# Performance work log

Hardware: AMD Instinct MI355X
Metric: run time of the kernel (lower is better)

Reference implementation:

```python
import jax, jax.numpy as jnp
import numpy as np

# gaussian_radial_function width: gamma = 1/(2*sigma^2), sigma = radii spacing (2/7)
GAMMA = 6.125


def setup_inputs() -> dict:
    key = jax.random.key(0)
    k1, k2, k3, k4, k5 = jax.random.split(key, 5)
    n, b, a, c, d, r = 4, 256, 256, 16, 16, 8
    inp = jax.random.normal(k1, (n, c, a), dtype=jnp.float32)
    difference_mat = jax.random.normal(k2, (n, b, a, 3), dtype=jnp.float32)
    relative_mask = jax.random.uniform(k3, (n, b, a), dtype=jnp.float32)
    W = jax.random.normal(k4, (d, c, r), dtype=jnp.float32) / np.float32(np.sqrt(c * r))
    radii = jax.random.uniform(k5, (r,), dtype=jnp.float32) * 2.0
    return {"input": inp, "difference_mat": difference_mat,
            "relative_mask": relative_mask, "W": W, "radii": radii}


def reference(input, difference_mat, relative_mask, W, radii):
    # distances |x_b - x_a|: [n, b, a]
    dist = jnp.sqrt(jnp.sum(difference_mat * difference_mat, axis=-1))
    # gaussian radial basis: [n, b, a, r]
    R = jnp.exp(-GAMMA * (dist[..., None] - radii) ** 2)
    # apply relative mask (kernel = mask[n,b,a] * kernel[d,c,n,b,a] in original)
    R = R * relative_mask[..., None]
    # kernel[d,c,n,b,a] = sum_r W[d,c,r] * R[n,b,a,r]; fused with the
    # contraction 'nca,dcnba->ndb' into a single einsum.
    return jnp.einsum('nca,dcr,nbar->ndb', input, W, R)
```

## Files before the change

### kernel.cpp

```cpp
#include <hip/hip_runtime.h>
#include <math.h>

constexpr int N = 4, B = 256, A = 256, C = 16, D = 16, RR = 8;
constexpr int DR = D * RR;
constexpr int BT = 4;
constexpr float GAMMA = 6.125f;

__global__ __launch_bounds__(256) void se3_compute_P(
    const float* __restrict__ input, const float* __restrict__ W,
    float* __restrict__ P)
{
    const int blk = blockIdx.x;
    const int n  = blk / DR;
    const int dr = blk % DR;
    const int d  = dr / RR;
    const int r  = dr % RR;
    const int a  = threadIdx.x;

    float s = 0.f;
#pragma unroll
    for (int c = 0; c < C; ++c) {
        s += W[(d * C + c) * RR + r] * input[(n * C + c) * A + a];
    }
    P[(size_t)blk * A + a] = s;
}

__global__ __launch_bounds__(256) void se3_compute_out(
    const float* __restrict__ P, const float* __restrict__ diff,
    const float* __restrict__ mask, const float* __restrict__ radii,
    float* __restrict__ out)
{
    const int blk = blockIdx.x;
    const int n  = blk / (B / BT);
    const int b0 = (blk % (B / BT)) * BT;
    const int a  = threadIdx.x;
    const int lane = threadIdx.x & 63;
    const int wave = threadIdx.x >> 6;

    float rad[RR];
#pragma unroll
    for (int r = 0; r < RR; ++r) rad[r] = radii[r];

    float preg[DR];
    const float* Pn = P + (size_t)n * DR * A + a;
#pragma unroll
    for (int dr = 0; dr < DR; ++dr) preg[dr] = Pn[dr * A];

    __shared__ float lds[BT][4][D];

#pragma unroll
    for (int bi = 0; bi < BT; ++bi) {
        const int b = b0 + bi;
        const size_t nba = (size_t)(n * B + b) * A + a;
        const float* dp = diff + nba * 3;
        const float dx = dp[0], dy = dp[1], dz = dp[2];
        const float dist = sqrtf(dx * dx + dy * dy + dz * dz);
        const float m = mask[nba];

        float R[RR];
#pragma unroll
        for (int r = 0; r < RR; ++r) {
            const float t = dist - rad[r];
            R[r] = m * __expf(-GAMMA * t * t);
        }

        float acc[D];
#pragma unroll
        for (int d = 0; d < D; ++d) {
            float s = 0.f;
#pragma unroll
            for (int r = 0; r < RR; ++r) s += R[r] * preg[d * RR + r];
            acc[d] = s;
        }

        {
            const bool hi32 = (lane & 32) != 0;
#pragma unroll
            for (int i = 0; i < 8; ++i) {
                float send = hi32 ? acc[i] : acc[i + 8];
                float recv = __shfl_xor(send, 32, 64);
                acc[i] = (hi32 ? acc[i + 8] : acc[i]) + recv;
            }
        }
        {
            const bool hi16 = (lane & 16) != 0;
#pragma unroll
            for (int i = 0; i < 4; ++i) {
                float send = hi16 ? acc[i] : acc[i + 4];
                float recv = __shfl_xor(send, 16, 64);
                acc[i] = (hi16 ? acc[i + 4] : acc[i]) + recv;
            }
        }
        {
            const bool hi8 = (lane & 8) != 0;
#pragma unroll
            for (int i = 0; i < 2; ++i) {
                float send = hi8 ? acc[i] : acc[i + 2];
                float recv = __shfl_xor(send, 8, 64);
                acc[i] = (hi8 ? acc[i + 2] : acc[i]) + recv;
            }
        }
        {
            const bool hi4 = (lane & 4) != 0;
            float send = hi4 ? acc[0] : acc[1];
            float recv = __shfl_xor(send, 4, 64);
            acc[0] = (hi4 ? acc[1] : acc[0]) + recv;
        }
        float v = acc[0];
        v += __shfl_xor(v, 1, 64);
        v += __shfl_xor(v, 2, 64);
        if ((lane & 3) == 0) lds[bi][wave][(lane >> 2) & 15] = v;
    }
    __syncthreads();

    if (threadIdx.x < BT * D) {
        const int bi = threadIdx.x / D;
        const int d  = threadIdx.x % D;
        const float s = lds[bi][0][d] + lds[bi][1][d] + lds[bi][2][d] + lds[bi][3][d];
        out[(n * D + d) * B + (b0 + bi)] = s;
    }
}

__global__ __launch_bounds__(256) void se3_fused(
    const float* __restrict__ input, const float* __restrict__ diff,
    const float* __restrict__ mask, const float* __restrict__ W,
    const float* __restrict__ radii, float* __restrict__ out)
{
    const int blk = blockIdx.x;
    const int n = blk / B;
    const int b = blk % B;
    const int a = threadIdx.x;

    __shared__ float Wl[D * C * RR];
    for (int i = threadIdx.x; i < D * C * RR; i += 256) Wl[i] = W[i];
    __syncthreads();

    const size_t nba = (size_t)(n * B + b) * A + a;
    const float* dp = diff + nba * 3;
    const float dx = dp[0], dy = dp[1], dz = dp[2];
    const float dist = sqrtf(dx * dx + dy * dy + dz * dz);
    const float m = mask[nba];

    float R[RR];
#pragma unroll
    for (int r = 0; r < RR; ++r) {
        const float t = dist - radii[r];
        R[r] = m * __expf(-GAMMA * t * t);
    }

    float acc[D];
#pragma unroll
    for (int d = 0; d < D; ++d) acc[d] = 0.f;
    for (int c = 0; c < C; ++c) {
        const float x = input[(n * C + c) * A + a];
        float xr[RR];
#pragma unroll
        for (int r = 0; r < RR; ++r) xr[r] = x * R[r];
#pragma unroll
        for (int d = 0; d < D; ++d) {
#pragma unroll
            for (int r = 0; r < RR; ++r)
                acc[d] += Wl[(d * C + c) * RR + r] * xr[r];
        }
    }

    __shared__ float lds[4 * D];
    const int lane = threadIdx.x & 63;
    const int wave = threadIdx.x >> 6;
#pragma unroll
    for (int d = 0; d < D; ++d) {
        float v = acc[d];
#pragma unroll
        for (int off = 32; off > 0; off >>= 1)
            v += __shfl_down(v, off, 64);
        if (lane == 0) lds[wave * D + d] = v;
    }
    __syncthreads();
    if (threadIdx.x < D) {
        const int d = threadIdx.x;
        const float s = lds[d] + lds[D + d] + lds[2 * D + d] + lds[3 * D + d];
        out[(n * D + d) * B + b] = s;
    }
}

extern "C" void kernel_launch(void* const* d_in, const int* in_sizes, int n_in,
                              void* d_out, int out_size, void* d_ws, size_t ws_size,
                              hipStream_t stream) {
    const float* input = (const float*)d_in[0];
    const float* diff  = (const float*)d_in[1];
    const float* mask  = (const float*)d_in[2];
    const float* W     = (const float*)d_in[3];
    const float* radii = (const float*)d_in[4];
    float* out = (float*)d_out;

    const size_t needP = (size_t)N * DR * A * sizeof(float);
    if (ws_size >= needP) {
        float* P = (float*)d_ws;
        se3_compute_P<<<N * DR, 256, 0, stream>>>(input, W, P);
        se3_compute_out<<<N * (B / BT), 256, 0, stream>>>(P, diff, mask, radii, out);
    } else {
        se3_fused<<<N * B, 256, 0, stream>>>(input, diff, mask, W, radii, out);
    }
}
```

Measured before the change: 16.12 us.

## Fuse P precompute into output kernel, recomputing W·input per block

Removes the separate kernel that wrote the P = W·input intermediate to workspace. Each block of the output kernel now recomputes its P values in registers from the input column and W. This saves one launch and a round trip of P through global memory. In exchange, every block redoes 2048 FMAs per thread and reads all of W through uniform loads, which adds register pressure on top of the 128-entry preg array.

```diff
diff --git a/kernel.cpp b/kernel.cpp
--- a/kernel.cpp
+++ b/kernel.cpp
@@ -6,29 +6,10 @@
 constexpr int BT = 4;
 constexpr float GAMMA = 6.125f;
 
-__global__ __launch_bounds__(256) void se3_compute_P(
-    const float* __restrict__ input, const float* __restrict__ W,
-    float* __restrict__ P)
-{
-    const int blk = blockIdx.x;
-    const int n  = blk / DR;
-    const int dr = blk % DR;
-    const int d  = dr / RR;
-    const int r  = dr % RR;
-    const int a  = threadIdx.x;
-
-    float s = 0.f;
-#pragma unroll
-    for (int c = 0; c < C; ++c) {
-        s += W[(d * C + c) * RR + r] * input[(n * C + c) * A + a];
-    }
-    P[(size_t)blk * A + a] = s;
-}
-
-__global__ __launch_bounds__(256) void se3_compute_out(
-    const float* __restrict__ P, const float* __restrict__ diff,
-    const float* __restrict__ mask, const float* __restrict__ radii,
-    float* __restrict__ out)
+__global__ __launch_bounds__(256) void se3_fused_all(
+    const float* __restrict__ input, const float* __restrict__ diff,
+    const float* __restrict__ mask, const float* __restrict__ W,
+    const float* __restrict__ radii, float* __restrict__ out)
 {
     const int blk = blockIdx.x;
     const int n  = blk / (B / BT);
@@ -37,14 +18,30 @@
     const int lane = threadIdx.x & 63;
     const int wave = threadIdx.x >> 6;
 
+    float x[C];
+#pragma unroll
+    for (int c = 0; c < C; ++c) x[c] = input[(n * C + c) * A + a];
+
     float rad[RR];
 #pragma unroll
     for (int r = 0; r < RR; ++r) rad[r] = radii[r];
 
     float preg[DR];
-    const float* Pn = P + (size_t)n * DR * A + a;
 #pragma unroll
-    for (int dr = 0; dr < DR; ++dr) preg[dr] = Pn[dr * A];
+    for (int d = 0; d < D; ++d) {
+        float acc[RR];
+#pragma unroll
+        for (int r = 0; r < RR; ++r) acc[r] = 0.f;
+#pragma unroll
+        for (int c = 0; c < C; ++c) {
+            const float xc = x[c];
+            const float* Wdc = W + (d * C + c) * RR;
+#pragma unroll
+            for (int r = 0; r < RR; ++r) acc[r] += Wdc[r] * xc;
+        }
+#pragma unroll
+        for (int r = 0; r < RR; ++r) preg[d * RR + r] = acc[r];
+    }
 
     __shared__ float lds[BT][4][D];
 
@@ -121,68 +118,6 @@
     }
 }
 
-__global__ __launch_bounds__(256) void se3_fused(
-    const float* __restrict__ input, const float* __restrict__ diff,
-    const float* __restrict__ mask, const float* __restrict__ W,
-    const float* __restrict__ radii, float* __restrict__ out)
-{
-    const int blk = blockIdx.x;
-    const int n = blk / B;
-    const int b = blk % B;
-    const int a = threadIdx.x;
-
-    __shared__ float Wl[D * C * RR];
-    for (int i = threadIdx.x; i < D * C * RR; i += 256) Wl[i] = W[i];
-    __syncthreads();
-
-    const size_t nba = (size_t)(n * B + b) * A + a;
-    const float* dp = diff + nba * 3;
-    const float dx = dp[0], dy = dp[1], dz = dp[2];
-    const float dist = sqrtf(dx * dx + dy * dy + dz * dz);
-    const float m = mask[nba];
-
-    float R[RR];
-#pragma unroll
-    for (int r = 0; r < RR; ++r) {
-        const float t = dist - radii[r];
-        R[r] = m * __expf(-GAMMA * t * t);
-    }
-
-    float acc[D];
-#pragma unroll
-    for (int d = 0; d < D; ++d) acc[d] = 0.f;
-    for (int c = 0; c < C; ++c) {
-        const float x = input[(n * C + c) * A + a];
-        float xr[RR];
-#pragma unroll
-        for (int r = 0; r < RR; ++r) xr[r] = x * R[r];
-#pragma unroll
-        for (int d = 0; d < D; ++d) {
-#pragma unroll
-            for (int r = 0; r < RR; ++r)
-                acc[d] += Wl[(d * C + c) * RR + r] * xr[r];
-        }
-    }
-
-    __shared__ float lds[4 * D];
-    const int lane = threadIdx.x & 63;
-    const int wave = threadIdx.x >> 6;
-#pragma unroll
-    for (int d = 0; d < D; ++d) {
-        float v = acc[d];
-#pragma unroll
-        for (int off = 32; off > 0; off >>= 1)
-            v += __shfl_down(v, off, 64);
-        if (lane == 0) lds[wave * D + d] = v;
-    }
-    __syncthreads();
-    if (threadIdx.x < D) {
-        const int d = threadIdx.x;
-        const float s = lds[d] + lds[D + d] + lds[2 * D + d] + lds[3 * D + d];
-        out[(n * D + d) * B + b] = s;
-    }
-}
-
 extern "C" void kernel_launch(void* const* d_in, const int* in_sizes, int n_in,
                               void* d_out, int out_size, void* d_ws, size_t ws_size,
                               hipStream_t stream) {
@@ -193,12 +128,5 @@
     const float* radii = (const float*)d_in[4];
     float* out = (float*)d_out;
 
-    const size_t needP = (size_t)N * DR * A * sizeof(float);
-    if (ws_size >= needP) {
-        float* P = (float*)d_ws;
-        se3_compute_P<<<N * DR, 256, 0, stream>>>(input, W, P);
-        se3_compute_out<<<N * (B / BT), 256, 0, stream>>>(P, diff, mask, radii, out);
-    } else {
-        se3_fused<<<N * B, 256, 0, stream>>>(input, diff, mask, W, radii, out);
-    }
+    se3_fused_all<<<N * (B / BT), 256, 0, stream>>>(input, diff, mask, W, radii, out);
 }
```

After: 19.60 us. 21.6% more time.

## Transpose P to [n][a][dr] and split D across two thread halves

Applied to the files above, without the earlier changes.

The precomputed P tensor is stored a-major with dr contiguous, so each thread reads a contiguous run of values. se3_compute_out now runs 512 threads per block, and each half handles 8 of the 16 d outputs. This halves the per-thread P register array and is meant to raise occupancy and latency hiding. In exchange, each half recomputes the distance, mask and exponentials for the same (b, a), and the cross-lane reduction and LDS layout are adjusted to match.

```diff
diff --git a/kernel.cpp b/kernel.cpp
--- a/kernel.cpp
+++ b/kernel.cpp
@@ -11,21 +11,23 @@
     float* __restrict__ P)
 {
     const int blk = blockIdx.x;
-    const int n  = blk / DR;
-    const int dr = blk % DR;
-    const int d  = dr / RR;
-    const int r  = dr % RR;
-    const int a  = threadIdx.x;
+    const int n  = blk >> 7;
+    const int a2 = blk & 127;
+    const int al = threadIdx.x >> 7;
+    const int dr = threadIdx.x & 127;
+    const int a  = a2 * 2 + al;
+    const int d  = dr >> 3;
+    const int r  = dr & 7;
 
     float s = 0.f;
 #pragma unroll
     for (int c = 0; c < C; ++c) {
         s += W[(d * C + c) * RR + r] * input[(n * C + c) * A + a];
     }
-    P[(size_t)blk * A + a] = s;
-}
-
-__global__ __launch_bounds__(256) void se3_compute_out(
+    P[((size_t)(n * A) + a) * DR + dr] = s;
+}
+
+__global__ __launch_bounds__(512) void se3_compute_out(
     const float* __restrict__ P, const float* __restrict__ diff,
     const float* __restrict__ mask, const float* __restrict__ radii,
     float* __restrict__ out)
@@ -33,7 +35,8 @@
     const int blk = blockIdx.x;
     const int n  = blk / (B / BT);
     const int b0 = (blk % (B / BT)) * BT;
-    const int a  = threadIdx.x;
+    const int h  = threadIdx.x >> 8;
+    const int a  = threadIdx.x & 255;
     const int lane = threadIdx.x & 63;
     const int wave = threadIdx.x >> 6;
 
@@ -41,12 +44,12 @@
 #pragma unroll
     for (int r = 0; r < RR; ++r) rad[r] = radii[r];
 
-    float preg[DR];
-    const float* Pn = P + (size_t)n * DR * A + a;
-#pragma unroll
-    for (int dr = 0; dr < DR; ++dr) preg[dr] = Pn[dr * A];
-
-    __shared__ float lds[BT][4][D];
+    float preg[DR / 2];
+    const float* Pt = P + ((size_t)(n * A) + a) * DR + h * (DR / 2);
+#pragma unroll
+    for (int j = 0; j < DR / 2; ++j) preg[j] = Pt[j];
+
+    __shared__ float lds[BT][8][8];
 
 #pragma unroll
     for (int bi = 0; bi < BT; ++bi) {
@@ -64,59 +67,54 @@
             R[r] = m * __expf(-GAMMA * t * t);
         }
 
-        float acc[D];
-#pragma unroll
-        for (int d = 0; d < D; ++d) {
+        float acc[8];
+#pragma unroll
+        for (int dl = 0; dl < 8; ++dl) {
             float s = 0.f;
 #pragma unroll
-            for (int r = 0; r < RR; ++r) s += R[r] * preg[d * RR + r];
-            acc[d] = s;
+            for (int r = 0; r < RR; ++r) s += R[r] * preg[dl * RR + r];
+            acc[dl] = s;
         }
 
         {
-            const bool hi32 = (lane & 32) != 0;
-#pragma unroll
-            for (int i = 0; i < 8; ++i) {
-                float send = hi32 ? acc[i] : acc[i + 8];
+            const bool hi = (lane & 32) != 0;
+#pragma unroll
+            for (int i = 0; i < 4; ++i) {
+                float send = hi ? acc[i] : acc[i + 4];
                 float recv = __shfl_xor(send, 32, 64);
-                acc[i] = (hi32 ? acc[i + 8] : acc[i]) + recv;
+                acc[i] = (hi ? acc[i + 4] : acc[i]) + recv;
             }
         }
         {
-            const bool hi16 = (lane & 16) != 0;
-#pragma unroll
-            for (int i = 0; i < 4; ++i) {
-                float send = hi16 ? acc[i] : acc[i + 4];
+            const bool hi = (lane & 16) != 0;
+#pragma unroll
+            for (int i = 0; i < 2; ++i) {
+                float send = hi ? acc[i] : acc[i + 2];
                 float recv = __shfl_xor(send, 16, 64);
-                acc[i] = (hi16 ? acc[i + 4] : acc[i]) + recv;
+                acc[i] = (hi ? acc[i + 2] : acc[i]) + recv;
             }
         }
         {
-            const bool hi8 = (lane & 8) != 0;
-#pragma unroll
-            for (int i = 0; i < 2; ++i) {
-                float send = hi8 ? acc[i] : acc[i + 2];
-                float recv = __shfl_xor(send, 8, 64);
-                acc[i] = (hi8 ? acc[i + 2] : acc[i]) + recv;
-            }
-        }
-        {
-            const bool hi4 = (lane & 4) != 0;
-            float send = hi4 ? acc[0] : acc[1];
-            float recv = __shfl_xor(send, 4, 64);
-            acc[0] = (hi4 ? acc[1] : acc[0]) + recv;
+            const bool hi = (lane & 8) != 0;
+            float send = hi ? acc[0] : acc[1];
+            float recv = __shfl_xor(send, 8, 64);
+            acc[0] = (hi ? acc[1] : acc[0]) + recv;
         }
         float v = acc[0];
         v += __shfl_xor(v, 1, 64);
         v += __shfl_xor(v, 2, 64);
-        if ((lane & 3) == 0) lds[bi][wave][(lane >> 2) & 15] = v;
+        v += __shfl_xor(v, 4, 64);
+        if ((lane & 7) == 0) lds[bi][wave][(lane >> 3) & 7] = v;
     }
     __syncthreads();
 
     if (threadIdx.x < BT * D) {
-        const int bi = threadIdx.x / D;
-        const int d  = threadIdx.x % D;
-        const float s = lds[bi][0][d] + lds[bi][1][d] + lds[bi][2][d] + lds[bi][3][d];
+        const int bi = threadIdx.x >> 4;
+        const int d  = threadIdx.x & 15;
+        const int hh = d >> 3;
+        const int dl = d & 7;
+        const float s = lds[bi][hh * 4 + 0][dl] + lds[bi][hh * 4 + 1][dl]
+                      + lds[bi][hh * 4 + 2][dl] + lds[bi][hh * 4 + 3][dl];
         out[(n * D + d) * B + (b0 + bi)] = s;
     }
 }
@@ -164,7 +162,7 @@
         }
     }
 
-    __shared__ float lds[4 * D];
+    __shared__ float lds2[4 * D];
     const int lane = threadIdx.x & 63;
     const int wave = threadIdx.x >> 6;
 #pragma unroll
@@ -173,12 +171,12 @@
 #pragma unroll
         for (int off = 32; off > 0; off >>= 1)
             v += __shfl_down(v, off, 64);
-        if (lane == 0) lds[wave * D + d] = v;
+        if (lane == 0) lds2[wave * D + d] = v;
     }
     __syncthreads();
     if (threadIdx.x < D) {
         const int d = threadIdx.x;
-        const float s = lds[d] + lds[D + d] + lds[2 * D + d] + lds[3 * D + d];
+        const float s = lds2[d] + lds2[D + d] + lds2[2 * D + d] + lds2[3 * D + d];
         out[(n * D + d) * B + b] = s;
     }
 }
@@ -193,11 +191,11 @@
     const float* radii = (const float*)d_in[4];
     float* out = (float*)d_out;
 
-    const size_t needP = (size_t)N * DR * A * sizeof(float);
+    const size_t needP = (size_t)N * A * DR * sizeof(float);
     if (ws_size >= needP) {
         float* P = (float*)d_ws;
-        se3_compute_P<<<N * DR, 256, 0, stream>>>(input, W, P);
-        se3_compute_out<<<N * (B / BT), 256, 0, stream>>>(P, diff, mask, radii, out);
+        se3_compute_P<<<N * (A / 2), 256, 0, stream>>>(input, W, P);
+        se3_compute_out<<<N * (B / BT), 512, 0, stream>>>(P, diff, mask, radii, out);
     } else {
         se3_fused<<<N * B, 256, 0, stream>>>(input, diff, mask, W, radii, out);
     }
```

Measured after the change: 17.61 us. 1.09x slower.
